# Performance work log

Hardware: AMD Instinct MI355X
Metric: run time of the kernel (lower is better)

The kernel has to match this reference:

```python
import jax, jax.numpy as jnp
import numpy as np

STRIDE = 4

_LENGTHS = np.array([131070, 131074, 131069, 131075, 131072, 131071, 131073, 131072], dtype=np.int64)
assert _LENGTHS.sum() == 1048576


def setup_inputs() -> dict:
    key = jax.random.key(0)
    k1, k2, k3, k4 = jax.random.split(key, 4)
    N = int(_LENGTHS.sum())
    C_in, C_out = 96, 192
    feat = jax.random.normal(k1, (N, C_in), dtype=jnp.float32)
    coord = jax.random.normal(k2, (N, 3), dtype=jnp.float32)
    scores = jax.random.uniform(k3, (N,), dtype=jnp.float32)
    W = jax.random.normal(k4, (C_in, C_out), dtype=jnp.float32) * (1.0 / np.sqrt(C_in))
    b = jnp.zeros((C_out,), dtype=jnp.float32)
    lengths = jnp.asarray(_LENGTHS)
    batch = jnp.asarray(np.repeat(np.arange(len(_LENGTHS), dtype=np.int64), _LENGTHS))
    return {"feat": feat, "coord": coord, "scores": scores, "W": W, "b": b,
            "lengths": lengths, "batch": batch}


def _window_segments(lengths_np, batch):
    # per-point window-segment id for ragged windowed pooling
    offsets = np.concatenate([[0], np.cumsum(lengths_np)])          # [B+1]
    n_win = -(-lengths_np // STRIDE)                                 # ceil(L/stride), [B]
    win_off = np.concatenate([[0], np.cumsum(n_win)])                # [B+1]
    N = int(offsets[-1])
    M = int(win_off[-1])
    pos = jnp.arange(N) - jnp.asarray(offsets)[batch]                # position within batch
    seg = jnp.asarray(win_off)[batch] + pos // STRIDE                # [N] segment id
    return seg, M, n_win


def reference(feat, coord, scores, W, b, lengths, batch):
    lengths_np = np.asarray(lengths)
    seg, M, n_win = _window_segments(lengths_np, batch)
    counts = jax.ops.segment_sum(jnp.ones(feat.shape[0], feat.dtype), seg, num_segments=M)
    inv = 1.0 / counts
    # mean pooling per window (segment reduce), single pass over the data
    feat_down = jax.ops.segment_sum(feat, seg, num_segments=M) * inv[:, None]
    coord_down = jax.ops.segment_sum(coord, seg, num_segments=M) * inv[:, None]
    scores_down = jax.ops.segment_sum(scores, seg, num_segments=M) * inv
    batch_down = jnp.asarray(np.repeat(np.arange(len(lengths_np), dtype=np.int64), n_win))
    # proj + (Identity norm) + ReLU
    feat_out = jax.nn.relu(feat_down @ W + b)
    lengths_down = jnp.asarray(n_win)
    offset_down = jnp.cumsum(lengths_down)
    return feat_out, coord_down, batch_down, scores_down, lengths_down, offset_down
```

## Files before the change

### kernel.cpp

```cpp
#include <hip/hip_runtime.h>

#define CIN 96
#define COUT 192
#define SW 4
#define BM 128
#define KPA 96
#define KPW 104
#define TPB_A 256
#define TPT_A 8
#define TPB_B 512

typedef __attribute__((ext_vector_type(8))) short bf16x8;
typedef __attribute__((ext_vector_type(4))) float f32x4;

__device__ __forceinline__ short f2bf(float x) {
  unsigned int u;
  __builtin_memcpy(&u, &x, 4);
  u += 0x7fffu + ((u >> 16) & 1u);
  return (short)(u >> 16);
}

__global__ __launch_bounds__(TPB_A) void pool_kernel(
    const float* __restrict__ feat, const float* __restrict__ coord,
    const float* __restrict__ scores, const float* __restrict__ W,
    const int* __restrict__ lengths, int B,
    short* __restrict__ wsA, short* __restrict__ wsWt,
    float* __restrict__ out) {
  int M = 0;
  for (int i = 0; i < B; ++i) M += (lengths[i] + (SW - 1)) >> 2;
  const int R0 = M * 24;
  const int R1 = R0 + M;
  const int R2 = R1 + COUT * 12;

  const int base = blockIdx.x * (TPB_A * TPT_A) + threadIdx.x;

  #pragma unroll
  for (int u = 0; u < TPT_A; ++u) {
    const int t = base + u * TPB_A;
    if (t < R0) {
      const int w = t / 24;
      const int g = t - w * 24;
      int off = 0, woff = 0, st = 0, cw = 0;
      for (int i = 0; i < B; ++i) {
        const int L = lengths[i];
        const int nw = (L + (SW - 1)) >> 2;
        if (w >= woff && w < woff + nw) {
          st = off + (w - woff) * SW;
          const int rem = off + L - st;
          cw = rem < SW ? rem : SW;
        }
        off += L; woff += nw;
      }
      const float* fp = feat + (long long)st * CIN + g * 4;
      float4 v0 = *(const float4*)(fp);
      float4 v1 = *(const float4*)(fp + CIN);
      float4 v2 = *(const float4*)(fp + 2 * CIN);
      float4 v3 = *(const float4*)(fp + 3 * CIN);
      const float k1 = (cw > 1) ? 1.f : 0.f;
      const float k2 = (cw > 2) ? 1.f : 0.f;
      const float k3 = (cw > 3) ? 1.f : 0.f;
      float sx = v0.x + k1 * v1.x + k2 * v2.x + k3 * v3.x;
      float sy = v0.y + k1 * v1.y + k2 * v2.y + k3 * v3.y;
      float sz = v0.z + k1 * v1.z + k2 * v2.z + k3 * v3.z;
      float sw2 = v0.w + k1 * v1.w + k2 * v2.w + k3 * v3.w;
      const float inv = 1.0f / (float)cw;
      short4 h;
      h.x = f2bf(sx * inv); h.y = f2bf(sy * inv);
      h.z = f2bf(sz * inv); h.w = f2bf(sw2 * inv);
      *(short4*)&wsA[(long long)w * CIN + g * 4] = h;
    } else if (t < R1) {
      const int m = t - R0;
      int off = 0, woff = 0, st = 0, cw = 0, bf = 0;
      for (int i = 0; i < B; ++i) {
        const int L = lengths[i];
        const int nw = (L + (SW - 1)) >> 2;
        if (m >= woff && m < woff + nw) {
          st = off + (m - woff) * SW;
          const int rem = off + L - st;
          cw = rem < SW ? rem : SW;
          bf = i;
        }
        off += L; woff += nw;
      }
      const float* cp = coord + (long long)st * 3;
      const float* sp = scores + st;
      float cx = 0.f, cy = 0.f, cz = 0.f, ss = 0.f;
      #pragma unroll
      for (int p = 0; p < 4; ++p) {
        const float mk = (p < cw) ? 1.f : 0.f;
        cx = fmaf(mk, cp[p * 3 + 0], cx);
        cy = fmaf(mk, cp[p * 3 + 1], cy);
        cz = fmaf(mk, cp[p * 3 + 2], cz);
        ss = fmaf(mk, sp[p], ss);
      }
      const float inv = 1.0f / (float)cw;
      const long long o1 = (long long)M * COUT;
      const long long o2 = o1 + (long long)M * 3;
      const long long o3 = o2 + M;
      out[o1 + (long long)m * 3 + 0] = cx * inv;
      out[o1 + (long long)m * 3 + 1] = cy * inv;
      out[o1 + (long long)m * 3 + 2] = cz * inv;
      out[o2 + m] = (float)bf;
      out[o3 + m] = ss * inv;
    } else if (t < R2) {
      const int j = t - R1;
      const int kg = j / COUT;
      const int n = j - kg * COUT;
      const float* wp = W + (long long)kg * 8 * COUT + n;
      bf16x8 hv;
      #pragma unroll
      for (int q = 0; q < 8; ++q) hv[q] = f2bf(wp[q * COUT]);
      *(bf16x8*)&wsWt[n * KPW + kg * 8] = hv;
    }
  }

  if (blockIdx.x == 0 && threadIdx.x == 0) {
    const long long o4 = (long long)M * (COUT + 3 + 1 + 1);
    long long cum = 0;
    for (int i = 0; i < B; ++i) {
      const long long nw = ((long long)lengths[i] + (SW - 1)) >> 2;
      out[o4 + i] = (float)nw;
      cum += nw;
      out[o4 + B + i] = (float)cum;
    }
  }
}

__global__ __launch_bounds__(TPB_B) void gemm_kernel(
    const short* __restrict__ wsA, const short* __restrict__ wsWt,
    const float* __restrict__ bias, const int* __restrict__ lengths, int B,
    float* __restrict__ out) {
  __shared__ alignas(16) short Wt_lds[COUT * KPW];

  int M = 0;
  for (int i = 0; i < B; ++i) M += (lengths[i] + (SW - 1)) >> 2;

  const int tid = threadIdx.x;
  const long long m0 = (long long)blockIdx.x * BM;
  const int wv = tid >> 6;
  const int lane = tid & 63;
  const int lm = lane & 15;
  const int quad = lane >> 4;

  bf16x8 af[3];
  const short* arow = wsA + (m0 + wv * 16 + lm) * CIN;
  #pragma unroll
  for (int ks = 0; ks < 3; ++ks)
    af[ks] = *(const bf16x8*)(arow + ks * 32 + quad * 8);

  const float4* src = (const float4*)wsWt;
  float4* dst = (float4*)Wt_lds;
  #pragma unroll
  for (int i = 0; i < 5; ++i) {
    const int idx = tid + TPB_B * i;
    if (idx < (COUT * KPW * 2 / 16)) dst[idx] = src[idx];
  }
  __syncthreads();

  f32x4 acc[12];
  #pragma unroll
  for (int nt = 0; nt < 12; ++nt) acc[nt] = (f32x4){0.f, 0.f, 0.f, 0.f};

  #pragma unroll
  for (int nt = 0; nt < 12; ++nt) {
    const int nrow = nt * 16 + lm;
    #pragma unroll
    for (int ks = 0; ks < 3; ++ks) {
      bf16x8 bfr = *(const bf16x8*)&Wt_lds[nrow * KPW + ks * 32 + quad * 8];
      acc[nt] = __builtin_amdgcn_mfma_f32_16x16x32_bf16(af[ks], bfr, acc[nt], 0, 0, 0);
    }
  }

  #pragma unroll
  for (int nt = 0; nt < 12; ++nt) {
    const int col = nt * 16 + lm;
    const float bv = bias[col];
    const long long rbase = m0 + wv * 16 + quad * 4;
    #pragma unroll
    for (int r = 0; r < 4; ++r) {
      const long long m = rbase + r;
      if (m < M) {
        const float x = acc[nt][r] + bv;
        out[m * COUT + col] = x > 0.f ? x : 0.f;
      }
    }
  }
}

__global__ __launch_bounds__(256) void fused_kernel(
    const float* __restrict__ feat, const float* __restrict__ coord,
    const float* __restrict__ scores, const float* __restrict__ W,
    const float* __restrict__ bias, const int* __restrict__ lengths, int B,
    float* __restrict__ out) {
  __shared__ short A_lds[BM * KPA];
  __shared__ short Wt_lds[COUT * KPW];
  __shared__ int s_meta[BM];

  const int tid = threadIdx.x;
  const long long m0 = (long long)blockIdx.x * BM;

  long long M = 0;
  for (int i = 0; i < B; ++i) M += ((long long)lengths[i] + (SW - 1)) >> 2;

  long long startL = 0; int cntL = 0, bfL = 0;
  if (tid < BM) {
    long long m = m0 + tid;
    long long off = 0, woff = 0;
    for (int i = 0; i < B; ++i) {
      long long L = lengths[i];
      long long nw = (L + (SW - 1)) >> 2;
      if (m >= woff && m < woff + nw) {
        long long st = off + (m - woff) * SW;
        long long rem = off + L - st;
        startL = st;
        cntL = (int)(rem < (long long)SW ? rem : (long long)SW);
        bfL = i;
      }
      off += L; woff += nw;
    }
    s_meta[tid] = (int)startL | (cntL << 28);
  }
  __syncthreads();

  #pragma unroll 4
  for (int i = 0; i < 12; ++i) {
    int task = tid + 256 * i;
    int w = task / 24;
    int g = task - w * 24;
    int mv = s_meta[w];
    int cw = (int)((unsigned)mv >> 28);
    int st = mv & 0x0FFFFFFF;
    const float* fp = feat + (long long)st * CIN + g * 4;
    float sx = 0.f, sy = 0.f, sz = 0.f, sw2 = 0.f;
    for (int p = 0; p < cw; ++p) {
      float4 v = *(const float4*)(fp + p * CIN);
      sx += v.x; sy += v.y; sz += v.z; sw2 += v.w;
    }
    float inv = cw ? 1.0f / (float)cw : 0.f;
    short4 h;
    h.x = f2bf(sx * inv); h.y = f2bf(sy * inv);
    h.z = f2bf(sz * inv); h.w = f2bf(sw2 * inv);
    *(short4*)&A_lds[w * KPA + g * 4] = h;
  }

  #pragma unroll 3
  for (int i = 0; i < 9; ++i) {
    int task = tid + 256 * i;
    int kg = task / COUT;
    int n = task - kg * COUT;
    const float* wp = W + kg * 8 * COUT + n;
    bf16x8 hv;
    #pragma unroll
    for (int j = 0; j < 8; ++j) hv[j] = f2bf(wp[j * COUT]);
    *(bf16x8*)&Wt_lds[n * KPW + kg * 8] = hv;
  }

  if (tid < BM) {
    long long m = m0 + tid;
    if (m < M) {
      float cx = 0.f, cy = 0.f, cz = 0.f, ss = 0.f;
      const float* cp = coord + startL * 3;
      for (int p = 0; p < cntL; ++p) {
        cx += cp[p * 3 + 0]; cy += cp[p * 3 + 1]; cz += cp[p * 3 + 2];
        ss += scores[startL + p];
      }
      float inv = 1.0f / (float)cntL;
      long long o1 = M * (long long)COUT;
      long long o2 = o1 + M * 3;
      long long o3 = o2 + M;
      out[o1 + m * 3 + 0] = cx * inv;
      out[o1 + m * 3 + 1] = cy * inv;
      out[o1 + m * 3 + 2] = cz * inv;
      out[o2 + m] = (float)bfL;
      out[o3 + m] = ss * inv;
    }
  }
  if (blockIdx.x == 0 && tid == 0) {
    long long o4 = M * (long long)(COUT + 3 + 1 + 1);
    long long cum = 0;
    for (int i = 0; i < B; ++i) {
      long long nw = ((long long)lengths[i] + (SW - 1)) >> 2;
      out[o4 + i] = (float)nw;
      cum += nw;
      out[o4 + B + i] = (float)cum;
    }
  }

  __syncthreads();

  const int wv = tid >> 6;
  const int lane = tid & 63;
  const int lm = lane & 15;
  const int quad = lane >> 4;

  bf16x8 af[2][3];
  #pragma unroll
  for (int mt = 0; mt < 2; ++mt)
    #pragma unroll
    for (int ks = 0; ks < 3; ++ks)
      af[mt][ks] = *(const bf16x8*)&A_lds[(wv * 32 + mt * 16 + lm) * KPA + ks * 32 + quad * 8];

  f32x4 acc[2][12];
  #pragma unroll
  for (int mt = 0; mt < 2; ++mt)
    #pragma unroll
    for (int nt = 0; nt < 12; ++nt)
      acc[mt][nt] = (f32x4){0.f, 0.f, 0.f, 0.f};

  #pragma unroll
  for (int nt = 0; nt < 12; ++nt) {
    const int nrow = nt * 16 + lm;
    #pragma unroll
    for (int ks = 0; ks < 3; ++ks) {
      bf16x8 bfr = *(const bf16x8*)&Wt_lds[nrow * KPW + ks * 32 + quad * 8];
      acc[0][nt] = __builtin_amdgcn_mfma_f32_16x16x32_bf16(af[0][ks], bfr, acc[0][nt], 0, 0, 0);
      acc[1][nt] = __builtin_amdgcn_mfma_f32_16x16x32_bf16(af[1][ks], bfr, acc[1][nt], 0, 0, 0);
    }
  }

  #pragma unroll
  for (int nt = 0; nt < 12; ++nt) {
    int col = nt * 16 + lm;
    float bv = bias[col];
    #pragma unroll
    for (int mt = 0; mt < 2; ++mt) {
      long long rbase = m0 + wv * 32 + mt * 16 + quad * 4;
      #pragma unroll
      for (int r = 0; r < 4; ++r) {
        long long m = rbase + r;
        if (m < M) {
          float x = acc[mt][nt][r] + bv;
          out[m * COUT + col] = x > 0.f ? x : 0.f;
        }
      }
    }
  }
}

extern "C" void kernel_launch(void* const* d_in, const int* in_sizes, int n_in,
                              void* d_out, int out_size, void* d_ws, size_t ws_size,
                              hipStream_t stream) {
  const float* feat    = (const float*)d_in[0];
  const float* coord   = (const float*)d_in[1];
  const float* scores  = (const float*)d_in[2];
  const float* W       = (const float*)d_in[3];
  const float* bias    = (const float*)d_in[4];
  const int*   lengths = (const int*)d_in[5];
  float* out = (float*)d_out;

  const int N = in_sizes[2];
  const int B = in_sizes[5];
  const int Mmax = N / SW + B;

  const int blocksB = (Mmax + BM - 1) / BM;
  const long long Mpad = (long long)blocksB * BM;
  const size_t A_bytes = (size_t)Mpad * CIN * sizeof(short);
  const size_t WT_bytes = (size_t)COUT * KPW * sizeof(short);

  if (ws_size >= A_bytes + WT_bytes) {
    short* wsA = (short*)d_ws;
    short* wsWt = (short*)((char*)d_ws + A_bytes);
    const long long Tmax = (long long)Mmax * 25 + COUT * 12;
    const int blocksA = (int)((Tmax + (long long)TPB_A * TPT_A - 1) /
                              ((long long)TPB_A * TPT_A));
    pool_kernel<<<blocksA, TPB_A, 0, stream>>>(feat, coord, scores, W, lengths,
                                               B, wsA, wsWt, out);
    gemm_kernel<<<blocksB, TPB_B, 0, stream>>>(wsA, wsWt, bias, lengths, B, out);
  } else {
    fused_kernel<<<blocksB, 256, 0, stream>>>(feat, coord, scores, W, bias,
                                              lengths, B, out);
  }
}
```

Baseline: 651.8 us.

## Swap MFMA operands for row-contiguous float4 stores; one work item per thread in pool

The GEMM kernel swaps the A and B operands of the MFMA so each lane holds four consecutive output columns of one row. The epilogue then writes with float4 stores and float4 bias loads instead of scattered scalar stores, aiming for fewer store instructions and better coalescing on the large output. Separately, the pool kernel drops its loop of 8 items per thread and launches one thread per item, which trades more blocks for less serial work and lower register pressure per thread.

After: 639.5 us. Within noise of the previous version (-1.9%).

```diff
diff --git a/kernel.cpp b/kernel.cpp
--- a/kernel.cpp
+++ b/kernel.cpp
@@ -7,7 +7,6 @@
 #define KPA 96
 #define KPW 104
 #define TPB_A 256
-#define TPT_A 8
 #define TPB_B 512
 
 typedef __attribute__((ext_vector_type(8))) short bf16x8;
@@ -32,89 +31,83 @@
   const int R1 = R0 + M;
   const int R2 = R1 + COUT * 12;
 
-  const int base = blockIdx.x * (TPB_A * TPT_A) + threadIdx.x;
-
-  #pragma unroll
-  for (int u = 0; u < TPT_A; ++u) {
-    const int t = base + u * TPB_A;
-    if (t < R0) {
-      const int w = t / 24;
-      const int g = t - w * 24;
-      int off = 0, woff = 0, st = 0, cw = 0;
-      for (int i = 0; i < B; ++i) {
-        const int L = lengths[i];
-        const int nw = (L + (SW - 1)) >> 2;
-        if (w >= woff && w < woff + nw) {
-          st = off + (w - woff) * SW;
-          const int rem = off + L - st;
-          cw = rem < SW ? rem : SW;
-        }
-        off += L; woff += nw;
-      }
-      const float* fp = feat + (long long)st * CIN + g * 4;
-      float4 v0 = *(const float4*)(fp);
-      float4 v1 = *(const float4*)(fp + CIN);
-      float4 v2 = *(const float4*)(fp + 2 * CIN);
-      float4 v3 = *(const float4*)(fp + 3 * CIN);
-      const float k1 = (cw > 1) ? 1.f : 0.f;
-      const float k2 = (cw > 2) ? 1.f : 0.f;
-      const float k3 = (cw > 3) ? 1.f : 0.f;
-      float sx = v0.x + k1 * v1.x + k2 * v2.x + k3 * v3.x;
-      float sy = v0.y + k1 * v1.y + k2 * v2.y + k3 * v3.y;
-      float sz = v0.z + k1 * v1.z + k2 * v2.z + k3 * v3.z;
-      float sw2 = v0.w + k1 * v1.w + k2 * v2.w + k3 * v3.w;
-      const float inv = 1.0f / (float)cw;
-      short4 h;
-      h.x = f2bf(sx * inv); h.y = f2bf(sy * inv);
-      h.z = f2bf(sz * inv); h.w = f2bf(sw2 * inv);
-      *(short4*)&wsA[(long long)w * CIN + g * 4] = h;
-    } else if (t < R1) {
-      const int m = t - R0;
-      int off = 0, woff = 0, st = 0, cw = 0, bf = 0;
-      for (int i = 0; i < B; ++i) {
-        const int L = lengths[i];
-        const int nw = (L + (SW - 1)) >> 2;
-        if (m >= woff && m < woff + nw) {
-          st = off + (m - woff) * SW;
-          const int rem = off + L - st;
-          cw = rem < SW ? rem : SW;
-          bf = i;
-        }
-        off += L; woff += nw;
-      }
-      const float* cp = coord + (long long)st * 3;
-      const float* sp = scores + st;
-      float cx = 0.f, cy = 0.f, cz = 0.f, ss = 0.f;
-      #pragma unroll
-      for (int p = 0; p < 4; ++p) {
-        const float mk = (p < cw) ? 1.f : 0.f;
-        cx = fmaf(mk, cp[p * 3 + 0], cx);
-        cy = fmaf(mk, cp[p * 3 + 1], cy);
-        cz = fmaf(mk, cp[p * 3 + 2], cz);
-        ss = fmaf(mk, sp[p], ss);
-      }
-      const float inv = 1.0f / (float)cw;
-      const long long o1 = (long long)M * COUT;
-      const long long o2 = o1 + (long long)M * 3;
-      const long long o3 = o2 + M;
-      out[o1 + (long long)m * 3 + 0] = cx * inv;
-      out[o1 + (long long)m * 3 + 1] = cy * inv;
-      out[o1 + (long long)m * 3 + 2] = cz * inv;
-      out[o2 + m] = (float)bf;
-      out[o3 + m] = ss * inv;
-    } else if (t < R2) {
-      const int j = t - R1;
-      const int kg = j / COUT;
-      const int n = j - kg * COUT;
-      const float* wp = W + (long long)kg * 8 * COUT + n;
-      bf16x8 hv;
-      #pragma unroll
-      for (int q = 0; q < 8; ++q) hv[q] = f2bf(wp[q * COUT]);
-      *(bf16x8*)&wsWt[n * KPW + kg * 8] = hv;
-    }
-  }
-
-  if (blockIdx.x == 0 && threadIdx.x == 0) {
+  const int t = blockIdx.x * TPB_A + threadIdx.x;
+
+  if (t < R0) {
+    const int w = t / 24;
+    const int g = t - w * 24;
+    int off = 0, woff = 0, st = 0, cw = 0;
+    for (int i = 0; i < B; ++i) {
+      const int L = lengths[i];
+      const int nw = (L + (SW - 1)) >> 2;
+      if (w >= woff && w < woff + nw) {
+        st = off + (w - woff) * SW;
+        const int rem = off + L - st;
+        cw = rem < SW ? rem : SW;
+      }
+      off += L; woff += nw;
+    }
+    const float* fp = feat + (long long)st * CIN + g * 4;
+    float4 v0 = *(const float4*)(fp);
+    float4 v1 = *(const float4*)(fp + CIN);
+    float4 v2 = *(const float4*)(fp + 2 * CIN);
+    float4 v3 = *(const float4*)(fp + 3 * CIN);
+    const float k1 = (cw > 1) ? 1.f : 0.f;
+    const float k2 = (cw > 2) ? 1.f : 0.f;
+    const float k3 = (cw > 3) ? 1.f : 0.f;
+    const float inv = 1.0f / (float)cw;
+    short4 h;
+    h.x = f2bf((v0.x + k1 * v1.x + k2 * v2.x + k3 * v3.x) * inv);
+    h.y = f2bf((v0.y + k1 * v1.y + k2 * v2.y + k3 * v3.y) * inv);
+    h.z = f2bf((v0.z + k1 * v1.z + k2 * v2.z + k3 * v3.z) * inv);
+    h.w = f2bf((v0.w + k1 * v1.w + k2 * v2.w + k3 * v3.w) * inv);
+    *(short4*)&wsA[(long long)w * CIN + g * 4] = h;
+  } else if (t < R1) {
+    const int m = t - R0;
+    int off = 0, woff = 0, st = 0, cw = 0, bf = 0;
+    for (int i = 0; i < B; ++i) {
+      const int L = lengths[i];
+      const int nw = (L + (SW - 1)) >> 2;
+      if (m >= woff && m < woff + nw) {
+        st = off + (m - woff) * SW;
+        const int rem = off + L - st;
+        cw = rem < SW ? rem : SW;
+        bf = i;
+      }
+      off += L; woff += nw;
+    }
+    const float* cp = coord + (long long)st * 3;
+    const float* sp = scores + st;
+    float cx = 0.f, cy = 0.f, cz = 0.f, ss = 0.f;
+    #pragma unroll
+    for (int p = 0; p < 4; ++p) {
+      const float mk = (p < cw) ? 1.f : 0.f;
+      cx = fmaf(mk, cp[p * 3 + 0], cx);
+      cy = fmaf(mk, cp[p * 3 + 1], cy);
+      cz = fmaf(mk, cp[p * 3 + 2], cz);
+      ss = fmaf(mk, sp[p], ss);
+    }
+    const float inv = 1.0f / (float)cw;
+    const long long o1 = (long long)M * COUT;
+    const long long o2 = o1 + (long long)M * 3;
+    const long long o3 = o2 + M;
+    out[o1 + (long long)m * 3 + 0] = cx * inv;
+    out[o1 + (long long)m * 3 + 1] = cy * inv;
+    out[o1 + (long long)m * 3 + 2] = cz * inv;
+    out[o2 + m] = (float)bf;
+    out[o3 + m] = ss * inv;
+  } else if (t < R2) {
+    const int j = t - R1;
+    const int kg = j / COUT;
+    const int n = j - kg * COUT;
+    const float* wp = W + (long long)kg * 8 * COUT + n;
+    bf16x8 hv;
+    #pragma unroll
+    for (int q = 0; q < 8; ++q) hv[q] = f2bf(wp[q * COUT]);
+    *(bf16x8*)&wsWt[n * KPW + kg * 8] = hv;
+  }
+
+  if (t == 0) {
     const long long o4 = (long long)M * (COUT + 3 + 1 + 1);
     long long cum = 0;
     for (int i = 0; i < B; ++i) {
@@ -167,22 +160,23 @@
     #pragma unroll
     for (int ks = 0; ks < 3; ++ks) {
       bf16x8 bfr = *(const bf16x8*)&Wt_lds[nrow * KPW + ks * 32 + quad * 8];
-      acc[nt] = __builtin_amdgcn_mfma_f32_16x16x32_bf16(af[ks], bfr, acc[nt], 0, 0, 0);
-    }
-  }
-
-  #pragma unroll
-  for (int nt = 0; nt < 12; ++nt) {
-    const int col = nt * 16 + lm;
-    const float bv = bias[col];
-    const long long rbase = m0 + wv * 16 + quad * 4;
-    #pragma unroll
-    for (int r = 0; r < 4; ++r) {
-      const long long m = rbase + r;
-      if (m < M) {
-        const float x = acc[nt][r] + bv;
-        out[m * COUT + col] = x > 0.f ? x : 0.f;
-      }
+      acc[nt] = __builtin_amdgcn_mfma_f32_16x16x32_bf16(bfr, af[ks], acc[nt], 0, 0, 0);
+    }
+  }
+
+  const long long m = m0 + wv * 16 + lm;
+  if (m < M) {
+    float* orow = out + m * COUT;
+    #pragma unroll
+    for (int nt = 0; nt < 12; ++nt) {
+      const int c0 = nt * 16 + quad * 4;
+      const float4 bv = *(const float4*)&bias[c0];
+      float4 o;
+      o.x = acc[nt][0] + bv.x; o.x = o.x > 0.f ? o.x : 0.f;
+      o.y = acc[nt][1] + bv.y; o.y = o.y > 0.f ? o.y : 0.f;
+      o.z = acc[nt][2] + bv.z; o.z = o.z > 0.f ? o.z : 0.f;
+      o.w = acc[nt][3] + bv.w; o.w = o.w > 0.f ? o.w : 0.f;
+      *(float4*)&orow[c0] = o;
     }
   }
 }
@@ -361,8 +355,7 @@
     short* wsA = (short*)d_ws;
     short* wsWt = (short*)((char*)d_ws + A_bytes);
     const long long Tmax = (long long)Mmax * 25 + COUT * 12;
-    const int blocksA = (int)((Tmax + (long long)TPB_A * TPT_A - 1) /
-                              ((long long)TPB_A * TPT_A));
+    const int blocksA = (int)((Tmax + TPB_A - 1) / TPB_A);
     pool_kernel<<<blocksA, TPB_A, 0, stream>>>(feat, coord, scores, W, lengths,
                                                B, wsA, wsWt, out);
     gemm_kernel<<<blocksB, TPB_B, 0, stream>>>(wsA, wsWt, bias, lengths, B, out);
```
